# Kernel optimization log

Measured on AMD Instinct MI355X. Metric: run time of the kernel, lower is better.

The kernel has to match this reference:

```python
import jax, jax.numpy as jnp
import numpy as np

B, N, D, C = 8, 400, 768, 3
K = 0.4
# Original keeps ranked positions whose argsort value (original index) < k*N.
# That count is static: M = #{j in [0,N) : j < k*N}
M = int(np.sum(np.arange(N) < K * N))  # 160
# static off-diagonal pair index lists (i != j), row-major like the nested loops
_ii, _jj = np.nonzero(~np.eye(M, dtype=bool))
II = jnp.asarray(_ii)
JJ = jnp.asarray(_jj)


def setup_inputs() -> dict:
    key = jax.random.key(0)
    k1, k2, k3, k4 = jax.random.split(key, 4)
    x = jax.random.normal(k1, (B, N, D), dtype=jnp.float32)
    w_span = jax.random.normal(k2, (D, 1), dtype=jnp.float32) * 0.02
    b_span = jnp.zeros((1,), dtype=jnp.float32)
    w_pair = jax.random.normal(k3, (3 * D, C), dtype=jnp.float32) * 0.02
    b_pair = jnp.zeros((C,), dtype=jnp.float32)
    span_ranges = jax.random.randint(k4, (N, 2), 0, 40, dtype=jnp.int32)
    return {"x": x, "w_span": w_span, "b_span": b_span,
            "w_pair": w_pair, "b_pair": b_pair, "span_ranges": span_ranges}


def reference(x, w_span, b_span, w_pair, b_pair, span_ranges):
    # span scorer: Linear(D,1) + sigmoid -> [B, N]
    h = jax.nn.sigmoid(x @ w_span + b_span)[..., 0]
    # torch.argsort(descending=True)
    order = jnp.argsort(-h, axis=-1)  # [B, N], original span indices in rank order
    # keep ranked positions j where order[b, j] < k*N (exactly M per row)
    pos = jnp.sort(jnp.where(order < K * N, jnp.arange(N), N), axis=-1)[:, :M]  # [B, M]
    # gather selected spans (built under no_grad in the original)
    x_ranked = jax.lax.stop_gradient(jnp.take_along_axis(x, pos[:, :, None], axis=1))  # [B, M, D]
    ranges_ranked = span_ranges[pos]  # [B, M, 2]

    # pair scorer decomposed over the concat [x_i, x_j, x_i*x_j]
    w1, w2, w3 = w_pair[:D], w_pair[D:2 * D], w_pair[2 * D:]
    a = x_ranked @ w1  # [B, M, C] contribution of x_i
    b = x_ranked @ w2  # [B, M, C] contribution of x_j
    mult = x_ranked[:, :, None, :] * x_ranked[:, None, :, :]  # [B, M, M, D]
    logits = a[:, :, None, :] + b[:, None, :, :] + mult @ w3 + b_pair  # [B, M, M, C]
    probs = jax.nn.softmax(jax.nn.sigmoid(logits), axis=-1)

    pair_probs = probs[:, II, JJ]  # [B, M*(M-1), C], off-diagonal pairs
    pair_ranges = jnp.stack([ranges_ranked[:, II], ranges_ranked[:, JJ]], axis=2)  # [B, P, 2, 2]
    return pair_probs, pair_ranges
```

## Files before the change

### kernel.cpp

```cpp
#include <hip/hip_runtime.h>
#include <math.h>

constexpr int B_ = 8;
constexpr int N_ = 400;
constexpr int D_ = 768;
constexpr int M_ = 160;
constexpr int PAIRS_ = M_ * (M_ - 1);
constexpr size_t BMD_ = (size_t)B_ * M_ * D_;
constexpr int NT_ = M_ / 16;
constexpr int TRI_ = NT_ * (NT_ + 1) / 2;

typedef __attribute__((ext_vector_type(8))) short short8;
typedef __attribute__((ext_vector_type(4))) float floatx4;


__device__ __forceinline__ unsigned cvt_pk_bf16(float lo, float hi) {
  unsigned r;
  asm("v_cvt_pk_bf16_f32 %0, %1, %2" : "=v"(r) : "v"(lo), "v"(hi));
  return r;
}

__global__ __launch_bounds__(256) void k_span(const float* __restrict__ x,
                                              const float* __restrict__ w_span,
                                              double* __restrict__ z) {
  int row = blockIdx.x * 4 + (threadIdx.x >> 6);
  int lane = threadIdx.x & 63;
  const float* xr = x + (size_t)row * D_;
  double acc = 0.0;
#pragma unroll
  for (int it = 0; it < 3; ++it) {
    int d = it * 256 + lane * 4;
    float4 xv = *(const float4*)(xr + d);
    float4 wv = *(const float4*)(w_span + d);
    acc += (double)xv.x * wv.x + (double)xv.y * wv.y +
           (double)xv.z * wv.z + (double)xv.w * wv.w;
  }
#pragma unroll
  for (int off = 32; off > 0; off >>= 1)
    acc += __shfl_down(acc, off, 64);
  if (lane == 0) z[row] = acc;
}

__global__ __launch_bounds__(256) void k_prep_rank(const float* __restrict__ x,
                                                   const float* __restrict__ w_pair,
                                                   const float* __restrict__ b_pair,
                                                   const double* __restrict__ z,
                                                   const int* __restrict__ span_ranges,
                                                   float* __restrict__ aterm,
                                                   float* __restrict__ bterm,
                                                   int* __restrict__ rr,
                                                   short* __restrict__ Xbf,
                                                   short* __restrict__ Ybf) {
  __shared__ double zsh[N_];
  __shared__ int ranksh[M_];
  __shared__ int pos_sh[M_];
  int blk = blockIdx.x;
  int b = blk / 40;
  int t = threadIdx.x;

  for (int j = t; j < N_; j += 256) zsh[j] = z[b * N_ + j];
  __syncthreads();
  if (t < M_) {
    double zi = zsh[t];
    int cnt = 0;
    for (int j = 0; j < N_; ++j) {
      double zj = zsh[j];
      cnt += (zj > zi) || (zj == zi && j < t);
    }
    ranksh[t] = cnt;
  }
  __syncthreads();
  if (t < M_) {
    int r = ranksh[t];
    int slot = 0;
#pragma unroll 8
    for (int k = 0; k < M_; ++k) slot += (ranksh[k] < r);
    pos_sh[slot] = r;
  }
  __syncthreads();

  int wid = t >> 6;
  int lane = t & 63;
  int i0 = (blk % 40) * 4 + wid;
  int s = b * M_ + i0;
  int row = pos_sh[i0];
  const float* xr = x + ((size_t)(b * N_ + row)) * D_;
  const float* w3 = w_pair + 2 * D_ * 3;

  float a0 = 0, a1 = 0, a2 = 0, c0 = 0, c1 = 0, c2 = 0;
#pragma unroll
  for (int it = 0; it < 3; ++it) {
    int d = it * 256 + lane * 4;
    float4 xv = *(const float4*)(xr + d);
    float xf[4] = {xv.x, xv.y, xv.z, xv.w};

    float w1v[12], w2v[12], w3v[12];
#pragma unroll
    for (int q = 0; q < 3; ++q) {
      *(float4*)(w1v + 4 * q) = *(const float4*)(w_pair + (size_t)d * 3 + 4 * q);
      *(float4*)(w2v + 4 * q) = *(const float4*)(w_pair + (size_t)(D_ + d) * 3 + 4 * q);
      *(float4*)(w3v + 4 * q) = *(const float4*)(w3 + (size_t)d * 3 + 4 * q);
    }
#pragma unroll
    for (int e = 0; e < 4; ++e) {
      a0 += xf[e] * w1v[e * 3 + 0];
      a1 += xf[e] * w1v[e * 3 + 1];
      a2 += xf[e] * w1v[e * 3 + 2];
      c0 += xf[e] * w2v[e * 3 + 0];
      c1 += xf[e] * w2v[e * 3 + 1];
      c2 += xf[e] * w2v[e * 3 + 2];
    }

    size_t o = (size_t)s * D_ + d;
    uint2 xp;
    xp.x = cvt_pk_bf16(xf[0], xf[1]);
    xp.y = cvt_pk_bf16(xf[2], xf[3]);
    *(uint2*)(Xbf + o) = xp;
#pragma unroll
    for (int c = 0; c < 3; ++c) {
      uint2 yp;
      yp.x = cvt_pk_bf16(xf[0] * w3v[0 * 3 + c], xf[1] * w3v[1 * 3 + c]);
      yp.y = cvt_pk_bf16(xf[2] * w3v[2 * 3 + c], xf[3] * w3v[3 * 3 + c]);
      *(uint2*)(Ybf + (size_t)c * BMD_ + o) = yp;
    }
  }
#pragma unroll
  for (int off = 32; off > 0; off >>= 1) {
    a0 += __shfl_down(a0, off, 64);
    a1 += __shfl_down(a1, off, 64);
    a2 += __shfl_down(a2, off, 64);
    c0 += __shfl_down(c0, off, 64);
    c1 += __shfl_down(c1, off, 64);
    c2 += __shfl_down(c2, off, 64);
  }
  if (lane == 0) {
    aterm[s * 3 + 0] = a0 + b_pair[0];
    aterm[s * 3 + 1] = a1 + b_pair[1];
    aterm[s * 3 + 2] = a2 + b_pair[2];
    bterm[s * 3 + 0] = c0;
    bterm[s * 3 + 1] = c1;
    bterm[s * 3 + 2] = c2;
    *(int2*)(rr + s * 2) = *(const int2*)(span_ranges + row * 2);
  }
}

__global__ __launch_bounds__(256) void k_pairs(const short* __restrict__ Xbf,
                                               const short* __restrict__ Ybf,
                                               const float* __restrict__ aterm,
                                               const float* __restrict__ bterm,
                                               const int* __restrict__ rr,
                                               float* __restrict__ out_probs,
                                               float4* __restrict__ out_ranges) {
  int lane = threadIdx.x & 63;
  int w = blockIdx.x * 4 + (threadIdx.x >> 6);
  int b = w / TRI_;
  int t = w - b * TRI_;
  int ti = 0, rem = t;
  while (rem >= NT_ - ti) { rem -= NT_ - ti; ++ti; }
  int tj = ti + rem;
  int quad = lane >> 4;
  int l16 = lane & 15;

  size_t oa = ((size_t)(b * M_ + ti * 16 + l16)) * D_ + quad * 8;
  size_t ob = ((size_t)(b * M_ + tj * 16 + l16)) * D_ + quad * 8;

  const short* ah0 = Ybf + 0 * BMD_ + oa;
  const short* ah1 = Ybf + 1 * BMD_ + oa;
  const short* ah2 = Ybf + 2 * BMD_ + oa;
  const short* bhp = Xbf + ob;

  floatx4 acc0 = {0.f, 0.f, 0.f, 0.f};
  floatx4 acc1 = {0.f, 0.f, 0.f, 0.f};
  floatx4 acc2 = {0.f, 0.f, 0.f, 0.f};

#pragma unroll 6
  for (int k = 0; k < D_; k += 32) {
    short8 bh = *(const short8*)(bhp + k);
    short8 h0 = *(const short8*)(ah0 + k);
    short8 h1 = *(const short8*)(ah1 + k);
    short8 h2 = *(const short8*)(ah2 + k);
    acc0 = __builtin_amdgcn_mfma_f32_16x16x32_bf16(h0, bh, acc0, 0, 0, 0);
    acc1 = __builtin_amdgcn_mfma_f32_16x16x32_bf16(h1, bh, acc1, 0, 0, 0);
    acc2 = __builtin_amdgcn_mfma_f32_16x16x32_bf16(h2, bh, acc2, 0, 0, 0);
  }

  const float* at = aterm + (size_t)(b * M_) * 3;
  const float* bt = bterm + (size_t)(b * M_) * 3;
  const int* rrb = rr + (size_t)(b * M_) * 2;
  bool offdiag = (ti != tj);
  int j = tj * 16 + l16;
  float bj0 = bt[j * 3 + 0], bj1 = bt[j * 3 + 1], bj2 = bt[j * 3 + 2];
  float aj0 = at[j * 3 + 0], aj1 = at[j * 3 + 1], aj2 = at[j * 3 + 2];
  int rj0 = rrb[j * 2 + 0], rj1 = rrb[j * 2 + 1];

#pragma unroll
  for (int r = 0; r < 4; ++r) {
    int i = ti * 16 + quad * 4 + r;
    float ai0 = at[i * 3 + 0], ai1 = at[i * 3 + 1], ai2 = at[i * 3 + 2];
    int ri0 = rrb[i * 2 + 0], ri1 = rrb[i * 2 + 1];

    if (i != j) {
      float l0 = acc0[r] + ai0 + bj0;
      float l1 = acc1[r] + ai1 + bj1;
      float l2 = acc2[r] + ai2 + bj2;
      float s0 = 1.0f / (1.0f + expf(-l0));
      float s1 = 1.0f / (1.0f + expf(-l1));
      float s2 = 1.0f / (1.0f + expf(-l2));
      float e0 = expf(s0), e1 = expf(s1), e2 = expf(s2);
      float inv = 1.0f / (e0 + e1 + e2);
      int jj = j - (j > i ? 1 : 0);
      size_t p = (size_t)b * PAIRS_ + (size_t)i * (M_ - 1) + jj;
      out_probs[p * 3 + 0] = e0 * inv;
      out_probs[p * 3 + 1] = e1 * inv;
      out_probs[p * 3 + 2] = e2 * inv;
      float4 rg;
      rg.x = (float)ri0;
      rg.y = (float)ri1;
      rg.z = (float)rj0;
      rg.w = (float)rj1;
      out_ranges[p] = rg;
    }

    if (offdiag) {
      float bi0 = bt[i * 3 + 0], bi1 = bt[i * 3 + 1], bi2 = bt[i * 3 + 2];
      float l0 = acc0[r] + aj0 + bi0;
      float l1 = acc1[r] + aj1 + bi1;
      float l2 = acc2[r] + aj2 + bi2;
      float s0 = 1.0f / (1.0f + expf(-l0));
      float s1 = 1.0f / (1.0f + expf(-l1));
      float s2 = 1.0f / (1.0f + expf(-l2));
      float e0 = expf(s0), e1 = expf(s1), e2 = expf(s2);
      float inv = 1.0f / (e0 + e1 + e2);
      size_t p = (size_t)b * PAIRS_ + (size_t)j * (M_ - 1) + i;
      out_probs[p * 3 + 0] = e0 * inv;
      out_probs[p * 3 + 1] = e1 * inv;
      out_probs[p * 3 + 2] = e2 * inv;
      float4 rg;
      rg.x = (float)rj0;
      rg.y = (float)rj1;
      rg.z = (float)ri0;
      rg.w = (float)ri1;
      out_ranges[p] = rg;
    }
  }
}

extern "C" void kernel_launch(void* const* d_in, const int* in_sizes, int n_in,
                              void* d_out, int out_size, void* d_ws, size_t ws_size,
                              hipStream_t stream) {
  const float* x = (const float*)d_in[0];
  const float* w_span = (const float*)d_in[1];
  const float* w_pair = (const float*)d_in[3];
  const float* b_pair = (const float*)d_in[4];
  const int* span_ranges = (const int*)d_in[5];

  char* ws = (char*)d_ws;
  double* z = (double*)ws;
  float* aterm = (float*)(ws + 30720);
  float* bterm = (float*)(ws + 46080);
  int* rr = (int*)(ws + 61440);
  short* Xbf = (short*)(ws + 71680);
  short* Ybf = (short*)(ws + 2037760);

  float* out = (float*)d_out;
  float* out_probs = out;
  float4* out_ranges = (float4*)(out + (size_t)B_ * PAIRS_ * 3);

  k_span<<<(B_ * N_) / 4, 256, 0, stream>>>(x, w_span, z);
  k_prep_rank<<<(B_ * M_) / 4, 256, 0, stream>>>(x, w_pair, b_pair, z,
                                                 span_ranges, aterm, bterm,
                                                 rr, Xbf, Ybf);
  k_pairs<<<(B_ * TRI_) / 4, 256, 0, stream>>>(Xbf, Ybf, aterm, bterm, rr,
                                               out_probs, out_ranges);
}
```

Before: 108.6 us.

## Split pair-tile K reduction across two waves and parallelize rank counting

k_prep_rank now uses 512-thread blocks and spreads the O(N) rank count and the O(M) slot count across eight waves, combining partial counts through shared memory. Each block also handles twice as many rows, so there are half as many blocks and the rank work is repeated less often. k_pairs splits the D=768 reduction of each 16x16 tile between two waves that exchange accumulators through shared memory, and each wave then writes one of the two mirrored output halves. This aims to shorten the serial rank loop and give the pair kernel more parallelism and balanced epilogue work, at the cost of extra syncs and shared-memory traffic.

Result: faster. 92.57 us (-14.8%).

```diff
diff --git a/kernel.cpp b/kernel.cpp
--- a/kernel.cpp
+++ b/kernel.cpp
@@ -41,7 +41,7 @@
   if (lane == 0) z[row] = acc;
 }
 
-__global__ __launch_bounds__(256) void k_prep_rank(const float* __restrict__ x,
+__global__ __launch_bounds__(512) void k_prep_rank(const float* __restrict__ x,
                                                    const float* __restrict__ w_pair,
                                                    const float* __restrict__ b_pair,
                                                    const double* __restrict__ z,
@@ -52,36 +52,69 @@
                                                    short* __restrict__ Xbf,
                                                    short* __restrict__ Ybf) {
   __shared__ double zsh[N_];
+  __shared__ int cnt8[8][M_];
   __shared__ int ranksh[M_];
   __shared__ int pos_sh[M_];
   int blk = blockIdx.x;
-  int b = blk / 40;
+  int b = blk / 20;
   int t = threadIdx.x;
-
-  for (int j = t; j < N_; j += 256) zsh[j] = z[b * N_ + j];
+  int w = t >> 6;
+  int lane = t & 63;
+
+  if (t < N_) zsh[t] = z[b * N_ + t];
+  __syncthreads();
+
+  {
+    double zi0 = zsh[lane];
+    double zi1 = zsh[lane + 64];
+    double zi2 = (lane < 32) ? zsh[lane + 128] : 0.0;
+    int c0 = 0, c1 = 0, c2 = 0;
+    int jb = w * 50;
+    for (int q = 0; q < 50; ++q) {
+      int jg = jb + q;
+      double zj = zsh[jg];
+      c0 += (zj > zi0) || (zj == zi0 && jg < lane);
+      c1 += (zj > zi1) || (zj == zi1 && jg < lane + 64);
+      c2 += (zj > zi2) || (zj == zi2 && jg < lane + 128);
+    }
+    cnt8[w][lane] = c0;
+    cnt8[w][lane + 64] = c1;
+    if (lane < 32) cnt8[w][lane + 128] = c2;
+  }
   __syncthreads();
   if (t < M_) {
-    double zi = zsh[t];
-    int cnt = 0;
-    for (int j = 0; j < N_; ++j) {
-      double zj = zsh[j];
-      cnt += (zj > zi) || (zj == zi && j < t);
-    }
-    ranksh[t] = cnt;
+    int r = 0;
+#pragma unroll
+    for (int w2 = 0; w2 < 8; ++w2) r += cnt8[w2][t];
+    ranksh[t] = r;
+  }
+  __syncthreads();
+  {
+    int ri0 = ranksh[lane];
+    int ri1 = ranksh[lane + 64];
+    int ri2 = (lane < 32) ? ranksh[lane + 128] : 0;
+    int s0 = 0, s1 = 0, s2 = 0;
+    int kb = w * 20;
+    for (int q = 0; q < 20; ++q) {
+      int rk = ranksh[kb + q];
+      s0 += (rk < ri0);
+      s1 += (rk < ri1);
+      s2 += (rk < ri2);
+    }
+    cnt8[w][lane] = s0;
+    cnt8[w][lane + 64] = s1;
+    if (lane < 32) cnt8[w][lane + 128] = s2;
   }
   __syncthreads();
   if (t < M_) {
-    int r = ranksh[t];
-    int slot = 0;
-#pragma unroll 8
-    for (int k = 0; k < M_; ++k) slot += (ranksh[k] < r);
-    pos_sh[slot] = r;
-  }
-  __syncthreads();
-
-  int wid = t >> 6;
-  int lane = t & 63;
-  int i0 = (blk % 40) * 4 + wid;
+    int s = 0;
+#pragma unroll
+    for (int w2 = 0; w2 < 8; ++w2) s += cnt8[w2][t];
+    pos_sh[s] = ranksh[t];
+  }
+  __syncthreads();
+
+  int i0 = (blk % 20) * 8 + w;
   int s = b * M_ + i0;
   int row = pos_sh[i0];
   const float* xr = x + ((size_t)(b * N_ + row)) * D_;
@@ -151,18 +184,22 @@
                                                const int* __restrict__ rr,
                                                float* __restrict__ out_probs,
                                                float4* __restrict__ out_ranges) {
+  __shared__ float accx[12][4][64];
   int lane = threadIdx.x & 63;
-  int w = blockIdx.x * 4 + (threadIdx.x >> 6);
-  int b = w / TRI_;
-  int t = w - b * TRI_;
+  int wl = threadIdx.x >> 6;
+  int tl = wl >> 1;
+  int kh = wl & 1;
+  int tg = blockIdx.x * 2 + tl;
+  int b = tg / TRI_;
+  int t = tg - b * TRI_;
   int ti = 0, rem = t;
   while (rem >= NT_ - ti) { rem -= NT_ - ti; ++ti; }
   int tj = ti + rem;
   int quad = lane >> 4;
   int l16 = lane & 15;
 
-  size_t oa = ((size_t)(b * M_ + ti * 16 + l16)) * D_ + quad * 8;
-  size_t ob = ((size_t)(b * M_ + tj * 16 + l16)) * D_ + quad * 8;
+  size_t oa = ((size_t)(b * M_ + ti * 16 + l16)) * D_ + quad * 8 + kh * 384;
+  size_t ob = ((size_t)(b * M_ + tj * 16 + l16)) * D_ + quad * 8 + kh * 384;
 
   const short* ah0 = Ybf + 0 * BMD_ + oa;
   const short* ah1 = Ybf + 1 * BMD_ + oa;
@@ -173,8 +210,8 @@
   floatx4 acc1 = {0.f, 0.f, 0.f, 0.f};
   floatx4 acc2 = {0.f, 0.f, 0.f, 0.f};
 
-#pragma unroll 6
-  for (int k = 0; k < D_; k += 32) {
+#pragma unroll
+  for (int k = 0; k < 384; k += 32) {
     short8 bh = *(const short8*)(bhp + k);
     short8 h0 = *(const short8*)(ah0 + k);
     short8 h1 = *(const short8*)(ah1 + k);
@@ -184,25 +221,39 @@
     acc2 = __builtin_amdgcn_mfma_f32_16x16x32_bf16(h2, bh, acc2, 0, 0, 0);
   }
 
+#pragma unroll
+  for (int r = 0; r < 4; ++r) {
+    accx[r][wl][lane] = acc0[r];
+    accx[4 + r][wl][lane] = acc1[r];
+    accx[8 + r][wl][lane] = acc2[r];
+  }
+  __syncthreads();
+  int pw = wl ^ 1;
+#pragma unroll
+  for (int r = 0; r < 4; ++r) {
+    acc0[r] += accx[r][pw][lane];
+    acc1[r] += accx[4 + r][pw][lane];
+    acc2[r] += accx[8 + r][pw][lane];
+  }
+
+  bool diag = (ti == tj);
+  if (diag && kh == 1) return;
+
   const float* at = aterm + (size_t)(b * M_) * 3;
   const float* bt = bterm + (size_t)(b * M_) * 3;
   const int* rrb = rr + (size_t)(b * M_) * 2;
-  bool offdiag = (ti != tj);
   int j = tj * 16 + l16;
-  float bj0 = bt[j * 3 + 0], bj1 = bt[j * 3 + 1], bj2 = bt[j * 3 + 2];
-  float aj0 = at[j * 3 + 0], aj1 = at[j * 3 + 1], aj2 = at[j * 3 + 2];
   int rj0 = rrb[j * 2 + 0], rj1 = rrb[j * 2 + 1];
 
-#pragma unroll
-  for (int r = 0; r < 4; ++r) {
-    int i = ti * 16 + quad * 4 + r;
-    float ai0 = at[i * 3 + 0], ai1 = at[i * 3 + 1], ai2 = at[i * 3 + 2];
-    int ri0 = rrb[i * 2 + 0], ri1 = rrb[i * 2 + 1];
-
-    if (i != j) {
-      float l0 = acc0[r] + ai0 + bj0;
-      float l1 = acc1[r] + ai1 + bj1;
-      float l2 = acc2[r] + ai2 + bj2;
+  if (kh == 0) {
+    float bj0 = bt[j * 3 + 0], bj1 = bt[j * 3 + 1], bj2 = bt[j * 3 + 2];
+#pragma unroll
+    for (int r = 0; r < 4; ++r) {
+      int i = ti * 16 + quad * 4 + r;
+      if (i == j) continue;
+      float l0 = acc0[r] + at[i * 3 + 0] + bj0;
+      float l1 = acc1[r] + at[i * 3 + 1] + bj1;
+      float l2 = acc2[r] + at[i * 3 + 2] + bj2;
       float s0 = 1.0f / (1.0f + expf(-l0));
       float s1 = 1.0f / (1.0f + expf(-l1));
       float s2 = 1.0f / (1.0f + expf(-l2));
@@ -214,18 +265,20 @@
       out_probs[p * 3 + 1] = e1 * inv;
       out_probs[p * 3 + 2] = e2 * inv;
       float4 rg;
-      rg.x = (float)ri0;
-      rg.y = (float)ri1;
+      rg.x = (float)rrb[i * 2 + 0];
+      rg.y = (float)rrb[i * 2 + 1];
       rg.z = (float)rj0;
       rg.w = (float)rj1;
       out_ranges[p] = rg;
     }
-
-    if (offdiag) {
-      float bi0 = bt[i * 3 + 0], bi1 = bt[i * 3 + 1], bi2 = bt[i * 3 + 2];
-      float l0 = acc0[r] + aj0 + bi0;
-      float l1 = acc1[r] + aj1 + bi1;
-      float l2 = acc2[r] + aj2 + bi2;
+  } else {
+    float aj0 = at[j * 3 + 0], aj1 = at[j * 3 + 1], aj2 = at[j * 3 + 2];
+#pragma unroll
+    for (int r = 0; r < 4; ++r) {
+      int i = ti * 16 + quad * 4 + r;
+      float l0 = acc0[r] + aj0 + bt[i * 3 + 0];
+      float l1 = acc1[r] + aj1 + bt[i * 3 + 1];
+      float l2 = acc2[r] + aj2 + bt[i * 3 + 2];
       float s0 = 1.0f / (1.0f + expf(-l0));
       float s1 = 1.0f / (1.0f + expf(-l1));
       float s2 = 1.0f / (1.0f + expf(-l2));
@@ -238,8 +291,8 @@
       float4 rg;
       rg.x = (float)rj0;
       rg.y = (float)rj1;
-      rg.z = (float)ri0;
-      rg.w = (float)ri1;
+      rg.z = (float)rrb[i * 2 + 0];
+      rg.w = (float)rrb[i * 2 + 1];
       out_ranges[p] = rg;
     }
   }
@@ -267,9 +320,9 @@
   float4* out_ranges = (float4*)(out + (size_t)B_ * PAIRS_ * 3);
 
   k_span<<<(B_ * N_) / 4, 256, 0, stream>>>(x, w_span, z);
-  k_prep_rank<<<(B_ * M_) / 4, 256, 0, stream>>>(x, w_pair, b_pair, z,
-                                                 span_ranges, aterm, bterm,
-                                                 rr, Xbf, Ybf);
-  k_pairs<<<(B_ * TRI_) / 4, 256, 0, stream>>>(Xbf, Ybf, aterm, bterm, rr,
+  k_prep_rank<<<B_ * 20, 512, 0, stream>>>(x, w_pair, b_pair, z,
+                                           span_ranges, aterm, bterm,
+                                           rr, Xbf, Ybf);
+  k_pairs<<<(B_ * TRI_) / 2, 256, 0, stream>>>(Xbf, Ybf, aterm, bterm, rr,
                                                out_probs, out_ranges);
 }
```
